# Kernel optimization log

Measured on AMD Instinct MI355X. Metric: run time of the kernel, lower is better.

Reference implementation:

```python
import jax, jax.numpy as jnp
import numpy as np

B, N, M = 4, 4096, 4096
EPS = 1e-8
LOG_2PI = float(np.log(2.0 * 3.14159))  # module uses 3.14159, not math.pi


def setup_inputs() -> dict:
    key = jax.random.key(0)
    k1, k2, k3 = jax.random.split(key, 3)
    return {
        "pred_xyz": jax.random.normal(k1, (B, N, 3), dtype=jnp.float32),
        "pred_sigma": jax.random.uniform(k2, (B, N, 2), dtype=jnp.float32),
        "target": jax.random.normal(k3, (B, M, 3), dtype=jnp.float32),
    }


def reference(pred_xyz, pred_sigma, target):
    target_xyz = target[:, :, :3]
    # pairwise squared distances: [B, N, M]
    dist_xy = jnp.sum((pred_xyz[:, :, None, :2] - target_xyz[:, None, :, :2]) ** 2, axis=-1)
    dist_z = (pred_xyz[:, :, None, 2] - target_xyz[:, None, :, 2]) ** 2
    sigma_xy = pred_sigma[:, :, 0:1]  # [B, N, 1]
    sigma_z = pred_sigma[:, :, 1:2]   # [B, N, 1]
    log_coef = -jnp.log(sigma_xy + EPS) - 0.5 * jnp.log(sigma_z + EPS)  # [B, N, 1]
    log_probs = (log_coef - 1.5 * LOG_2PI
                 - 0.5 * dist_xy / (sigma_xy + EPS)
                 - 0.5 * dist_z / (sigma_z + EPS))  # [B, N, M]
    nll = -jax.nn.logsumexp(log_probs, axis=1)  # mixture over N predictions -> [B, M]
    return nll.mean()
```

## Files before the change

### kernel.cpp

```cpp
#include <hip/hip_runtime.h>


constexpr int Bc = 4, Nc = 4096, Mc = 4096;
constexpr int NSPLIT  = 8;
constexpr int NCHUNK  = Nc / NSPLIT;
constexpr int NTILES  = NCHUNK / 16;
constexpr int THREADS = 256;
constexpr int MBLK    = 64;
constexpr int REC     = 40;

#define EPS 1e-8f
constexpr float LOG2E   = 1.4426950408889634f;
constexpr float LN2     = 0.6931471805599453f;
constexpr float LOG_2PI = 1.8378762043478343f;
constexpr float K_CONST = -1.5f * LOG_2PI * LOG2E;

typedef __attribute__((ext_vector_type(8))) short bf16x8;
typedef __attribute__((ext_vector_type(4))) float f32x4;
typedef unsigned int   u32;
typedef unsigned short u16;

static __device__ __forceinline__ u16 f2bf(float x) {
    u32 u = __float_as_uint(x);
    return (u16)((u + 0x7fffu + ((u >> 16) & 1u)) >> 16);
}
static __device__ __forceinline__ float bf2f(u16 h) {
    return __uint_as_float((u32)h << 16);
}

__global__ __launch_bounds__(THREADS) void gmm_partial(
    const float* __restrict__ pred_xyz,
    const float* __restrict__ pred_sigma,
    const float* __restrict__ target,
    float* __restrict__ partials,
    float* __restrict__ out)
{
    __shared__ short lds[NCHUNK * REC];

    const int mblk = blockIdx.x;
    const int nck  = blockIdx.y;
    const int b    = blockIdx.z;
    const int tid  = threadIdx.x;

    if (mblk == 0 && nck == 0 && b == 0 && tid == 0) out[0] = 0.f;

    for (int t = tid; t < NCHUNK; t += THREADS) {
        const int n = nck * NCHUNK + t;
        const float* pp = pred_xyz + ((size_t)b * Nc + n) * 3;
        const float px = pp[0], py = pp[1], pz = pp[2];
        const float* ps = pred_sigma + ((size_t)b * Nc + n) * 2;
        const float sxy = ps[0] + EPS;
        const float sz  = ps[1] + EPS;
        const float A2 = -0.5f * LOG2E * __builtin_amdgcn_rcpf(sxy);
        const float C2 = -0.5f * LOG2E * __builtin_amdgcn_rcpf(sz);
        const float K2 = K_CONST - __builtin_amdgcn_logf(sxy)
                         - 0.5f * __builtin_amdgcn_logf(sz)
                         + A2 * (px * px + py * py) + C2 * (pz * pz);
        const float Bx = -2.f * A2 * px;
        const float By = -2.f * A2 * py;
        const float Cz = -2.f * C2 * pz;

        const u16 h0 = f2bf(K2), h1 = f2bf(A2), h2 = f2bf(C2),
                  h3 = f2bf(Bx), h4 = f2bf(By), h5 = f2bf(Cz);
        const u16 l0 = f2bf(K2 - bf2f(h0)), l1 = f2bf(A2 - bf2f(h1)),
                  l2 = f2bf(C2 - bf2f(h2)), l3 = f2bf(Bx - bf2f(h3)),
                  l4 = f2bf(By - bf2f(h4)), l5 = f2bf(Cz - bf2f(h5));

        const u32 d0 = (u32)h0 | ((u32)h1 << 16);
        const u32 d1 = (u32)h2 | ((u32)h3 << 16);
        const u32 d2 = (u32)h4 | ((u32)h5 << 16);
        const u32 e0 = (u32)l0 | ((u32)l1 << 16);
        const u32 e1 = (u32)l2 | ((u32)l3 << 16);
        const u32 e2 = (u32)l4 | ((u32)l5 << 16);
        u32* rec = (u32*)&lds[t * REC];
        rec[0] = d0; rec[1]  = d1; rec[2]  = d2;
        rec[3] = d0; rec[4]  = d1; rec[5]  = d2;
        rec[6] = e0; rec[7]  = e1; rec[8]  = e2;
        rec[9] = 0;  rec[10] = 0;  rec[11] = 0;
        rec[12] = 0; rec[13] = 0;  rec[14] = 0;  rec[15] = 0;
    }
    __syncthreads();

    const int lane = tid & 63;
    const int wave = tid >> 6;
    const int g    = lane >> 4;
    const int m    = mblk * MBLK + wave * 16 + (lane & 15);

    const float* tp = target + ((size_t)b * Mc + m) * 3;
    const float tx = tp[0], ty = tp[1], tz = tp[2];
    const float u1 = tx * tx + ty * ty, u2 = tz * tz;

    const u16 mh0 = f2bf(1.f), mh1 = f2bf(u1), mh2 = f2bf(u2),
              mh3 = f2bf(tx),  mh4 = f2bf(ty), mh5 = f2bf(tz);
    const u16 ml0 = 0,
              ml1 = f2bf(u1 - bf2f(mh1)), ml2 = f2bf(u2 - bf2f(mh2)),
              ml3 = f2bf(tx - bf2f(mh3)), ml4 = f2bf(ty - bf2f(mh4)),
              ml5 = f2bf(tz - bf2f(mh5));

    u16 s0, s1, s2, s3, s4, s5, s6, s7;
    if (g == 0)      { s0=mh0; s1=mh1; s2=mh2; s3=mh3; s4=mh4; s5=mh5; s6=ml0; s7=ml1; }
    else if (g == 1) { s0=ml2; s1=ml3; s2=ml4; s3=ml5; s4=mh0; s5=mh1; s6=mh2; s7=mh3; }
    else if (g == 2) { s0=mh4; s1=mh5; s2=0;   s3=0;   s4=0;   s5=0;   s6=0;   s7=0;   }
    else             { s0=0;   s1=0;   s2=0;   s3=0;   s4=0;   s5=0;   s6=0;   s7=0;   }
    bf16x8 bfrag;
    bfrag[0]=(short)s0; bfrag[1]=(short)s1; bfrag[2]=(short)s2; bfrag[3]=(short)s3;
    bfrag[4]=(short)s4; bfrag[5]=(short)s5; bfrag[6]=(short)s6; bfrag[7]=(short)s7;

    float a0 = 0.f, a1 = 0.f, a2 = 0.f, a3 = 0.f;
    const short* abase = &lds[(lane & 15) * REC + g * 8];
    const f32x4 zero4 = {0.f, 0.f, 0.f, 0.f};
#pragma unroll 4
    for (int it = 0; it < NTILES; ++it) {
        bf16x8 afrag = *(const bf16x8*)(abase + it * 16 * REC);
        f32x4 d = __builtin_amdgcn_mfma_f32_16x16x32_bf16(afrag, bfrag, zero4, 0, 0, 0);
        a0 += __builtin_amdgcn_exp2f(d[0]);
        a1 += __builtin_amdgcn_exp2f(d[1]);
        a2 += __builtin_amdgcn_exp2f(d[2]);
        a3 += __builtin_amdgcn_exp2f(d[3]);
    }

    float s = (a0 + a1) + (a2 + a3);
    s += __shfl_xor(s, 16, 64);
    s += __shfl_xor(s, 32, 64);
    if (g == 0)
        partials[((size_t)(b * NSPLIT + nck)) * Mc + m] = s;
}

__global__ __launch_bounds__(256) void gmm_finalize(
    const float* __restrict__ partials, float* __restrict__ out)
{
    const int t = blockIdx.x * 256 + threadIdx.x;
    const int b = t >> 12;
    const int m = t & (Mc - 1);

    float sum = 0.f;
#pragma unroll
    for (int c = 0; c < NSPLIT; ++c)
        sum += partials[((size_t)(b * NSPLIT + c)) * Mc + m];

    float local = __builtin_amdgcn_logf(sum);
#pragma unroll
    for (int off = 32; off > 0; off >>= 1)
        local += __shfl_down(local, off, 64);

    __shared__ float w[4];
    const int wave = threadIdx.x >> 6;
    if ((threadIdx.x & 63) == 0) w[wave] = local;
    __syncthreads();
    if (threadIdx.x == 0) {
        const float tot = w[0] + w[1] + w[2] + w[3];
        atomicAdd(out, -LN2 / (float)(Bc * Mc) * tot);
    }
}

extern "C" void kernel_launch(void* const* d_in, const int* in_sizes, int n_in,
                              void* d_out, int out_size, void* d_ws, size_t ws_size,
                              hipStream_t stream) {
    const float* pred_xyz   = (const float*)d_in[0];
    const float* pred_sigma = (const float*)d_in[1];
    const float* target     = (const float*)d_in[2];
    float* out      = (float*)d_out;
    float* partials = (float*)d_ws;

    dim3 grid(Mc / MBLK, NSPLIT, Bc);
    gmm_partial<<<grid, THREADS, 0, stream>>>(pred_xyz, pred_sigma, target,
                                              partials, out);
    gmm_finalize<<<Bc * Mc / 256, 256, 0, stream>>>(partials, out);
}
```

Measured before the change: 71.21 us.

## Fuse partial and finalize kernels with double-buffered record build over full N

Each block now loops over all N predictions in 512-point chunks, building the next chunk's LDS records while it computes on the current one (double buffering). The per-target log and block reduction happen in the same kernel, which removes the partials buffer and the finalize launch. The output is zeroed with a memset instead of inside the kernel. In exchange the grid drops from 2048 to 256 blocks, which lowers parallelism and occupancy (the doubled LDS also limits blocks per CU), and every block redoes the record preprocessing for all N.

Result: slower. 81.66 us (+14.7%).

```diff
diff --git a/kernel.cpp b/kernel.cpp
--- a/kernel.cpp
+++ b/kernel.cpp
@@ -2,11 +2,11 @@
 
 
 constexpr int Bc = 4, Nc = 4096, Mc = 4096;
-constexpr int NSPLIT  = 8;
-constexpr int NCHUNK  = Nc / NSPLIT;
-constexpr int NTILES  = NCHUNK / 16;
 constexpr int THREADS = 256;
 constexpr int MBLK    = 64;
+constexpr int NCK     = 512;
+constexpr int NCHUNKS = Nc / NCK;
+constexpr int CHT     = NCK / 16;
 constexpr int REC     = 40;
 
 #define EPS 1e-8f
@@ -28,24 +28,15 @@
     return __uint_as_float((u32)h << 16);
 }
 
-__global__ __launch_bounds__(THREADS) void gmm_partial(
+static __device__ __forceinline__ void build_records(
+    short* __restrict__ buf,
     const float* __restrict__ pred_xyz,
     const float* __restrict__ pred_sigma,
-    const float* __restrict__ target,
-    float* __restrict__ partials,
-    float* __restrict__ out)
+    int b, int n0, int tid)
 {
-    __shared__ short lds[NCHUNK * REC];
-
-    const int mblk = blockIdx.x;
-    const int nck  = blockIdx.y;
-    const int b    = blockIdx.z;
-    const int tid  = threadIdx.x;
-
-    if (mblk == 0 && nck == 0 && b == 0 && tid == 0) out[0] = 0.f;
-
-    for (int t = tid; t < NCHUNK; t += THREADS) {
-        const int n = nck * NCHUNK + t;
+#pragma unroll
+    for (int t = tid; t < NCK; t += THREADS) {
+        const int n = n0 + t;
         const float* pp = pred_xyz + ((size_t)b * Nc + n) * 3;
         const float px = pp[0], py = pp[1], pz = pp[2];
         const float* ps = pred_sigma + ((size_t)b * Nc + n) * 2;
@@ -72,20 +63,32 @@
         const u32 e0 = (u32)l0 | ((u32)l1 << 16);
         const u32 e1 = (u32)l2 | ((u32)l3 << 16);
         const u32 e2 = (u32)l4 | ((u32)l5 << 16);
-        u32* rec = (u32*)&lds[t * REC];
+        u32* rec = (u32*)&buf[t * REC];
         rec[0] = d0; rec[1]  = d1; rec[2]  = d2;
         rec[3] = d0; rec[4]  = d1; rec[5]  = d2;
         rec[6] = e0; rec[7]  = e1; rec[8]  = e2;
         rec[9] = 0;  rec[10] = 0;  rec[11] = 0;
         rec[12] = 0; rec[13] = 0;  rec[14] = 0;  rec[15] = 0;
     }
-    __syncthreads();
+}
 
+__global__ __launch_bounds__(THREADS) void gmm_fused(
+    const float* __restrict__ pred_xyz,
+    const float* __restrict__ pred_sigma,
+    const float* __restrict__ target,
+    float* __restrict__ out)
+{
+    __shared__ short lds[2 * NCK * REC];
+    __shared__ float wsum[4];
+
+    const int mblk = blockIdx.x;
+    const int b    = blockIdx.y;
+    const int tid  = threadIdx.x;
     const int lane = tid & 63;
     const int wave = tid >> 6;
     const int g    = lane >> 4;
-    const int m    = mblk * MBLK + wave * 16 + (lane & 15);
 
+    const int m = mblk * MBLK + wave * 16 + (lane & 15);
     const float* tp = target + ((size_t)b * Mc + m) * 3;
     const float tx = tp[0], ty = tp[1], tz = tp[2];
     const float u1 = tx * tx + ty * ty, u2 = tz * tz;
@@ -106,49 +109,40 @@
     bfrag[0]=(short)s0; bfrag[1]=(short)s1; bfrag[2]=(short)s2; bfrag[3]=(short)s3;
     bfrag[4]=(short)s4; bfrag[5]=(short)s5; bfrag[6]=(short)s6; bfrag[7]=(short)s7;
 
+    build_records(&lds[0], pred_xyz, pred_sigma, b, 0, tid);
+    __syncthreads();
+
     float a0 = 0.f, a1 = 0.f, a2 = 0.f, a3 = 0.f;
-    const short* abase = &lds[(lane & 15) * REC + g * 8];
     const f32x4 zero4 = {0.f, 0.f, 0.f, 0.f};
+    for (int ck = 0; ck < NCHUNKS; ++ck) {
+        if (ck + 1 < NCHUNKS)
+            build_records(&lds[((ck + 1) & 1) * (NCK * REC)],
+                          pred_xyz, pred_sigma, b, (ck + 1) * NCK, tid);
+
+        const short* base = &lds[(ck & 1) * (NCK * REC) + (lane & 15) * REC + g * 8];
 #pragma unroll 4
-    for (int it = 0; it < NTILES; ++it) {
-        bf16x8 afrag = *(const bf16x8*)(abase + it * 16 * REC);
-        f32x4 d = __builtin_amdgcn_mfma_f32_16x16x32_bf16(afrag, bfrag, zero4, 0, 0, 0);
-        a0 += __builtin_amdgcn_exp2f(d[0]);
-        a1 += __builtin_amdgcn_exp2f(d[1]);
-        a2 += __builtin_amdgcn_exp2f(d[2]);
-        a3 += __builtin_amdgcn_exp2f(d[3]);
+        for (int it = 0; it < CHT; ++it) {
+            bf16x8 afrag = *(const bf16x8*)(base + it * 16 * REC);
+            f32x4 d = __builtin_amdgcn_mfma_f32_16x16x32_bf16(afrag, bfrag, zero4, 0, 0, 0);
+            a0 += __builtin_amdgcn_exp2f(d[0]);
+            a1 += __builtin_amdgcn_exp2f(d[1]);
+            a2 += __builtin_amdgcn_exp2f(d[2]);
+            a3 += __builtin_amdgcn_exp2f(d[3]);
+        }
+        __syncthreads();
     }
 
     float s = (a0 + a1) + (a2 + a3);
     s += __shfl_xor(s, 16, 64);
     s += __shfl_xor(s, 32, 64);
-    if (g == 0)
-        partials[((size_t)(b * NSPLIT + nck)) * Mc + m] = s;
-}
-
-__global__ __launch_bounds__(256) void gmm_finalize(
-    const float* __restrict__ partials, float* __restrict__ out)
-{
-    const int t = blockIdx.x * 256 + threadIdx.x;
-    const int b = t >> 12;
-    const int m = t & (Mc - 1);
-
-    float sum = 0.f;
-#pragma unroll
-    for (int c = 0; c < NSPLIT; ++c)
-        sum += partials[((size_t)(b * NSPLIT + c)) * Mc + m];
-
-    float local = __builtin_amdgcn_logf(sum);
+    float contrib = (lane < 16) ? __builtin_amdgcn_logf(s) : 0.f;
 #pragma unroll
     for (int off = 32; off > 0; off >>= 1)
-        local += __shfl_down(local, off, 64);
-
-    __shared__ float w[4];
-    const int wave = threadIdx.x >> 6;
-    if ((threadIdx.x & 63) == 0) w[wave] = local;
+        contrib += __shfl_xor(contrib, off, 64);
+    if (lane == 0) wsum[wave] = contrib;
     __syncthreads();
-    if (threadIdx.x == 0) {
-        const float tot = w[0] + w[1] + w[2] + w[3];
+    if (tid == 0) {
+        const float tot = wsum[0] + wsum[1] + wsum[2] + wsum[3];
         atomicAdd(out, -LN2 / (float)(Bc * Mc) * tot);
     }
 }
@@ -159,11 +153,10 @@
     const float* pred_xyz   = (const float*)d_in[0];
     const float* pred_sigma = (const float*)d_in[1];
     const float* target     = (const float*)d_in[2];
-    float* out      = (float*)d_out;
-    float* partials = (float*)d_ws;
+    float* out = (float*)d_out;
 
-    dim3 grid(Mc / MBLK, NSPLIT, Bc);
-    gmm_partial<<<grid, THREADS, 0, stream>>>(pred_xyz, pred_sigma, target,
-                                              partials, out);
-    gmm_finalize<<<Bc * Mc / 256, 256, 0, stream>>>(partials, out);
+    hipMemsetAsync(out, 0, sizeof(float), stream);
+
+    dim3 grid(Mc / MBLK, Bc, 1);
+    gmm_fused<<<grid, THREADS, 0, stream>>>(pred_xyz, pred_sigma, target, out);
 }
```
